# Optimization experiments

Measured on AMD Instinct MI355X. Metric: run time of the kernel, lower is better.

The kernel has to match this reference:

```python
import jax, jax.numpy as jnp
import numpy as np

N, D = 8192, 512
LOGIT_SCALE = 2.659


def setup_inputs() -> dict:
    key = jax.random.key(0)
    k1, k2, k3 = jax.random.split(key, 3)
    text_features = jax.random.normal(k1, (N, D), dtype=jnp.float32)
    image_features = jax.random.normal(k2, (N, D), dtype=jnp.float32)
    labels = jax.random.randint(k3, (N,), 0, 100, dtype=jnp.int64)
    # sprinkle in some -1 (unlabeled) entries like the original supports
    labels = jnp.where(jax.random.uniform(jax.random.fold_in(key, 7), (N,)) < 0.1, -1, labels)
    return {"text_features": text_features, "image_features": image_features, "labels": labels}


def _l2_normalize(x):
    n = jnp.sqrt(jnp.sum(x * x, axis=-1, keepdims=True))
    return x / jnp.maximum(n, 1e-12)


def _soft_ce(s, t):
    # -(t * log softmax(s)).sum(-1) / t.sum(-1), averaged over rows
    loss = -jnp.sum(t * jax.nn.log_softmax(s, axis=-1), axis=-1)
    return jnp.mean(loss / jnp.sum(t, axis=-1))


def reference(text_features, image_features, labels):
    img = _l2_normalize(image_features)
    txt = _l2_normalize(text_features)
    logits_per_image = LOGIT_SCALE * (img @ txt.T)   # [N, N]
    logits_per_text = LOGIT_SCALE * (txt @ img.T)    # [N, N]

    # Vectorized equivalent of the per-row loop:
    # T[i,j] = 1 if i == j else (labels[i] == labels[j] and labels[i] != -1)
    eq = (labels[:, None] == labels[None, :]) & (labels[:, None] != -1)
    n = labels.shape[0]
    target = jnp.where(jnp.eye(n, dtype=bool), 1.0, eq.astype(jnp.float32))

    return (_soft_ce(logits_per_image, target) + _soft_ce(logits_per_text, target)) / 2
```

## Files before the change

### kernel.cpp

```cpp
#include <hip/hip_runtime.h>
#include <hip/hip_bf16.h>

#define N_ROWS 8192
#define DIM 512
#define SCALE 2.659f
#define MAXLOGIT 2.659f
#define LOG2E 1.4426950408889634f
#define NCHUNK 16
#define CHUNK 512
#define BM 128
#define BN 128
#define NCLS 128
#define GEMM_BLKS 1024

typedef __attribute__((ext_vector_type(8))) short short8;
typedef __attribute__((ext_vector_type(4))) float f32x4;

#define ZERO_F4 36896

__device__ __forceinline__ unsigned short f2bf(float f) {
    unsigned int u = __float_as_uint(f);
    u += 0x7fffu + ((u >> 16) & 1u);
    return (unsigned short)(u >> 16);
}

__global__ __launch_bounds__(256) void norm_cast_kernel(
    const float* __restrict__ text, const float* __restrict__ image,
    const int* __restrict__ labels,
    unsigned short* __restrict__ imgn, unsigned short* __restrict__ txtn,
    float4* __restrict__ zbase, float* __restrict__ sd, float* __restrict__ out)
{
    int zi = blockIdx.x * 256 + threadIdx.x;
    if (zi < ZERO_F4) zbase[zi] = make_float4(0.f, 0.f, 0.f, 0.f);
    if (zi == 0) out[0] = 0.f;

    int row  = blockIdx.x * 4 + (threadIdx.x >> 6);
    int lane = threadIdx.x & 63;
    const float4* si = (const float4*)(image + (size_t)row * DIM) + lane * 2;
    const float4* st = (const float4*)(text  + (size_t)row * DIM) + lane * 2;
    float4 a = si[0], b = si[1], c = st[0], d = st[1];
    float ssa = a.x*a.x + a.y*a.y + a.z*a.z + a.w*a.w
              + b.x*b.x + b.y*b.y + b.z*b.z + b.w*b.w;
    float sst = c.x*c.x + c.y*c.y + c.z*c.z + c.w*c.w
              + d.x*d.x + d.y*d.y + d.z*d.z + d.w*d.w;
    float sab = a.x*c.x + a.y*c.y + a.z*c.z + a.w*c.w
              + b.x*d.x + b.y*d.y + b.z*d.z + b.w*d.w;
    #pragma unroll
    for (int m = 1; m < 64; m <<= 1) {
        ssa += __shfl_xor(ssa, m, 64);
        sst += __shfl_xor(sst, m, 64);
        sab += __shfl_xor(sab, m, 64);
    }
    float sca = 1.0f / fmaxf(sqrtf(ssa), 1e-12f);
    float sct = 1.0f / fmaxf(sqrtf(sst), 1e-12f);
    uint4 oi, ot;
    oi.x = (unsigned)f2bf(a.x*sca) | ((unsigned)f2bf(a.y*sca) << 16);
    oi.y = (unsigned)f2bf(a.z*sca) | ((unsigned)f2bf(a.w*sca) << 16);
    oi.z = (unsigned)f2bf(b.x*sca) | ((unsigned)f2bf(b.y*sca) << 16);
    oi.w = (unsigned)f2bf(b.z*sca) | ((unsigned)f2bf(b.w*sca) << 16);
    ot.x = (unsigned)f2bf(c.x*sct) | ((unsigned)f2bf(c.y*sct) << 16);
    ot.y = (unsigned)f2bf(c.z*sct) | ((unsigned)f2bf(c.w*sct) << 16);
    ot.z = (unsigned)f2bf(d.x*sct) | ((unsigned)f2bf(d.y*sct) << 16);
    ot.w = (unsigned)f2bf(d.z*sct) | ((unsigned)f2bf(d.w*sct) << 16);
    *((uint4*)(imgn + (size_t)row * DIM) + lane) = oi;
    *((uint4*)(txtn + (size_t)row * DIM) + lane) = ot;
    if (lane == 0)
        sd[row] = (labels[row] < 0) ? sab * sca * sct : 0.0f;
}

#define ASYNC16(gp, lp) \
  __builtin_amdgcn_global_load_lds((const __attribute__((address_space(1))) void*)(gp), \
                                   (__attribute__((address_space(3))) void*)(lp), 16, 0, 0)

#define SFENCE __builtin_amdgcn_sched_barrier(0)

#define STAGE(b, tcol, k0)                                                    \
  {                                                                           \
    const unsigned short* Ap = A + (size_t)(rowBase + w*16 + srow) * DIM      \
                                 + (k0) + spsw;                               \
    const unsigned short* Bp = B + (size_t)((tcol) + w*16 + srow) * DIM       \
                                 + (k0) + spsw;                               \
    ASYNC16(Ap,            &Ald[b][(w*16) * 32]);                             \
    ASYNC16(Ap + 64 * DIM, &Ald[b][(64 + w*16) * 32]);                        \
    ASYNC16(Bp,            &Bld[b][(w*16) * 32]);                             \
    ASYNC16(Bp + 64 * DIM, &Bld[b][(64 + w*16) * 32]);                        \
  }

__global__ __launch_bounds__(256, 2) void gemm_fused_kernel(
    const unsigned short* __restrict__ imgn, const unsigned short* __restrict__ txtn,
    const int* __restrict__ labels,
    float* __restrict__ rs, float* __restrict__ cs,
    float* __restrict__ c_txt, float* __restrict__ c_img, int* __restrict__ cnt)
{
    __shared__ unsigned short Ald[4][BM * 32];
    __shared__ unsigned short Bld[4][BN * 32];
    __shared__ float red[2][BM];
    __shared__ float colb[2][CHUNK];
    __shared__ int   list[1024];
    __shared__ int   lcount;

    int tid  = threadIdx.x;

    if (blockIdx.x >= GEMM_BLKS) {
        int blk = blockIdx.x - GEMM_BLKS;
        int cls = blk & (NCLS - 1);
        int mat = (blk >> 7) & 1;
        int slc = blk >> 8;
        const unsigned* src = (const unsigned*)(mat ? imgn : txtn);
        float* dst = mat ? c_img : c_txt;
        if (tid == 0) lcount = 0;
        __syncthreads();
        int base0 = slc * 1024;
        #pragma unroll
        for (int it = 0; it < 4; ++it) {
            int i  = base0 + it * 256 + tid;
            int lb = labels[i];
            if (lb == cls) { int s = atomicAdd(&lcount, 1); list[s & 1023] = i; }
        }
        __syncthreads();
        int m = lcount;
        if (m == 0) return;
        if (mat == 0 && tid == 0) atomicAdd(&cnt[cls], m);
        float a0 = 0.f, a1 = 0.f;
        int r = 0;
        for (; r + 4 <= m; r += 4) {
            unsigned u0 = src[(size_t)list[r]   * (DIM/2) + tid];
            unsigned u1 = src[(size_t)list[r+1] * (DIM/2) + tid];
            unsigned u2 = src[(size_t)list[r+2] * (DIM/2) + tid];
            unsigned u3 = src[(size_t)list[r+3] * (DIM/2) + tid];
            a0 += __uint_as_float((u0 & 0xffffu) << 16) + __uint_as_float((u1 & 0xffffu) << 16)
                + __uint_as_float((u2 & 0xffffu) << 16) + __uint_as_float((u3 & 0xffffu) << 16);
            a1 += __uint_as_float(u0 & 0xffff0000u) + __uint_as_float(u1 & 0xffff0000u)
                + __uint_as_float(u2 & 0xffff0000u) + __uint_as_float(u3 & 0xffff0000u);
        }
        for (; r < m; ++r) {
            unsigned u = src[(size_t)list[r] * (DIM/2) + tid];
            a0 += __uint_as_float((u & 0xffffu) << 16);
            a1 += __uint_as_float(u & 0xffff0000u);
        }
        unsafeAtomicAdd(&dst[(size_t)cls * DIM + tid*2],     a0);
        unsafeAtomicAdd(&dst[(size_t)cls * DIM + tid*2 + 1], a1);
        return;
    }

    int bid    = blockIdx.x;
    int rowblk = bid & 63;
    int chunk  = bid >> 6;
    const unsigned short* A = imgn;
    const unsigned short* B = txtn;
    int rowBase  = rowblk * BM;
    int colBase0 = chunk * CHUNK;

    int lane = tid & 63;
    int w    = tid >> 6;
    int wr   = w >> 1, wc = w & 1;
    int q    = lane >> 4;
    int lm   = lane & 15;
    int qa   = q ^ ((lm >> 1) & 3);

    float s_acc[16];
    #pragma unroll
    for (int i = 0; i < 16; ++i) s_acc[i] = 0.f;

    int srow = lane >> 2;
    int spsw = (((lane & 3) ^ ((lane >> 3) & 3)) * 8);

    const float C1 = SCALE * LOG2E;
    const float C2 = -MAXLOGIT * LOG2E;

    STAGE(0, colBase0, 0);
    STAGE(1, colBase0, 32);
    SFENCE;
    asm volatile("s_waitcnt vmcnt(4)" ::: "memory");
    SFENCE;
    __builtin_amdgcn_s_barrier();
    SFENCE;

    #pragma unroll 1
    for (int tile = 0; tile < CHUNK / BN; ++tile) {
        f32x4 acc[4][4];
        #pragma unroll
        for (int mi = 0; mi < 4; ++mi)
          #pragma unroll
          for (int ni = 0; ni < 4; ++ni)
            acc[mi][ni] = (f32x4){0.f, 0.f, 0.f, 0.f};

        #pragma unroll
        for (int kt = 0; kt < DIM / 32; ++kt) {
            const int bcur = kt & 3;
            const int bpf  = (kt + 2) & 3;
            int g2 = tile * 16 + kt + 2;
            if (g2 < 64) {
                int t2 = g2 >> 4, k2 = g2 & 15;
                STAGE(bpf, colBase0 + t2 * BN, k2 * 32);
            }

            short8 af[4], bf[4];
            #pragma unroll
            for (int mi = 0; mi < 4; ++mi)
                af[mi] = *(const short8*)(&Ald[bcur][(wr*64 + mi*16 + lm)*32 + qa*8]);
            #pragma unroll
            for (int ni = 0; ni < 4; ++ni)
                bf[ni] = *(const short8*)(&Bld[bcur][(wc*64 + ni*16 + lm)*32 + qa*8]);
            #pragma unroll
            for (int mi = 0; mi < 4; ++mi)
              #pragma unroll
              for (int ni = 0; ni < 4; ++ni)
                acc[mi][ni] = __builtin_amdgcn_mfma_f32_16x16x32_bf16(
                                  af[mi], bf[ni], acc[mi][ni], 0, 0, 0);

            if (kt == DIM / 32 - 1) {
                #pragma unroll
                for (int ni = 0; ni < 4; ++ni) {
                    float csum = 0.f;
                    #pragma unroll
                    for (int mi = 0; mi < 4; ++mi) {
                      #pragma unroll
                      for (int r = 0; r < 4; ++r) {
                        float e = __builtin_amdgcn_exp2f(fmaf(acc[mi][ni][r], C1, C2));
                        s_acc[mi*4 + r] += e;
                        csum += e;
                      }
                    }
                    csum += __shfl_xor(csum, 16, 64);
                    csum += __shfl_xor(csum, 32, 64);
                    if (q == 0)
                        colb[wr][tile*BN + wc*64 + ni*16 + lm] = csum;
                }
            }

            SFENCE;
            if (g2 < 64) asm volatile("s_waitcnt vmcnt(4)" ::: "memory");
            else         asm volatile("s_waitcnt vmcnt(0)" ::: "memory");
            SFENCE;
            __builtin_amdgcn_s_barrier();
            SFENCE;
        }
    }

    #pragma unroll
    for (int idx = 0; idx < 16; ++idx) {
        float s = s_acc[idx];
        #pragma unroll
        for (int m = 1; m < 16; m <<= 1) s += __shfl_xor(s, m, 64);
        s_acc[idx] = s;
    }
    if (lm == 0) {
        #pragma unroll
        for (int idx = 0; idx < 16; ++idx) {
            int rl = wr*64 + (idx>>2)*16 + q*4 + (idx&3);
            red[wc][rl] = s_acc[idx];
        }
    }
    __syncthreads();
    if (tid < BM)
        unsafeAtomicAdd(&rs[rowBase + tid], red[0][tid] + red[1][tid]);
    for (int c = tid; c < CHUNK; c += 256)
        unsafeAtomicAdd(&cs[colBase0 + c], colb[0][c] + colb[1][c]);
}

__global__ __launch_bounds__(256) void loss_tail_kernel(
    const float* __restrict__ rs, const float* __restrict__ cs,
    const float* __restrict__ sd, const float* __restrict__ c_txt,
    const float* __restrict__ c_img, const int* __restrict__ cnt,
    float* __restrict__ out)
{
    __shared__ float wsum[4];
    int tid = threadIdx.x, lane = tid & 63, w = tid >> 6;
    int gidx = blockIdx.x * 256 + tid;
    float local;
    if (gidx < N_ROWS)
        local = (MAXLOGIT + logf(rs[gidx])) - 2.0f * SCALE * sd[gidx];
    else
        local = MAXLOGIT + logf(cs[gidx - N_ROWS]);

    int cls = blockIdx.x * 2 + (tid >> 7);
    int e0  = (tid & 127) * 4;
    int n   = cnt[cls];
    if (n > 0) {
        float4 x = *(const float4*)(c_txt + (size_t)cls * DIM + e0);
        float4 y = *(const float4*)(c_img + (size_t)cls * DIM + e0);
        float dotp = x.x*y.x + x.y*y.y + x.z*y.z + x.w*y.w;
        local -= 2.0f * SCALE * dotp / (float)n;
    }

    #pragma unroll
    for (int m = 1; m < 64; m <<= 1) local += __shfl_xor(local, m, 64);
    if (lane == 0) wsum[w] = local;
    __syncthreads();
    if (tid == 0)
        unsafeAtomicAdd(out, (wsum[0] + wsum[1] + wsum[2] + wsum[3])
                             * (1.0f / (2 * N_ROWS)));
}

extern "C" void kernel_launch(void* const* d_in, const int* in_sizes, int n_in,
                              void* d_out, int out_size, void* d_ws, size_t ws_size,
                              hipStream_t stream)
{
    const float* text   = (const float*)d_in[0];
    const float* image  = (const float*)d_in[1];
    const int*   labels = (const int*)d_in[2];

    unsigned short* imgn = (unsigned short*)d_ws;
    unsigned short* txtn = imgn + (size_t)N_ROWS * DIM;
    char* p = (char*)d_ws + 2 * (size_t)N_ROWS * DIM * sizeof(unsigned short);
    float* rs    = (float*)p;
    float* cs    = rs + N_ROWS;
    float* c_txt = cs + N_ROWS;
    float* c_img = c_txt + (size_t)NCLS * DIM;
    int*   cnt   = (int*)(c_img + (size_t)NCLS * DIM);
    float* sd    = (float*)(cnt + NCLS);
    float* out = (float*)d_out;

    hipLaunchKernelGGL(norm_cast_kernel, dim3(N_ROWS / 4), dim3(256), 0, stream,
                       text, image, labels, imgn, txtn, (float4*)rs, sd, out);
    hipLaunchKernelGGL(gemm_fused_kernel, dim3(GEMM_BLKS + 2048), dim3(256), 0, stream,
                       imgn, txtn, labels, rs, cs, c_txt, c_img, cnt);
    hipLaunchKernelGGL(loss_tail_kernel, dim3(64), dim3(256), 0, stream,
                       rs, cs, sd, c_txt, c_img, cnt, out);
}
```

Before: 167.4 us.

## Fuse loss tail into GEMM kernel via completion counter spin-wait

Removes the separate loss_tail kernel launch and folds its reduction into the GEMM/class-sum kernel. Every block bumps a global done counter after a threadfence. The first 64 blocks then spin on it with an acquire load until all blocks have finished, and only then compute the final loss. This saves one kernel launch and its inter-kernel gap. In exchange, 64 GEMM blocks keep their CU slots occupied while they wait, and the scheme depends on all blocks being co-schedulable or dispatched in order to avoid deadlock.

```diff
diff --git a/kernel.cpp b/kernel.cpp
--- a/kernel.cpp
+++ b/kernel.cpp
@@ -12,6 +12,7 @@
 #define BN 128
 #define NCLS 128
 #define GEMM_BLKS 1024
+#define TOTAL_BLKS 3072
 
 typedef __attribute__((ext_vector_type(8))) short short8;
 typedef __attribute__((ext_vector_type(4))) float f32x4;
@@ -28,11 +29,12 @@
     const float* __restrict__ text, const float* __restrict__ image,
     const int* __restrict__ labels,
     unsigned short* __restrict__ imgn, unsigned short* __restrict__ txtn,
-    float4* __restrict__ zbase, float* __restrict__ sd, float* __restrict__ out)
+    float4* __restrict__ zbase, float* __restrict__ sd,
+    int* __restrict__ done, float* __restrict__ out)
 {
     int zi = blockIdx.x * 256 + threadIdx.x;
     if (zi < ZERO_F4) zbase[zi] = make_float4(0.f, 0.f, 0.f, 0.f);
-    if (zi == 0) out[0] = 0.f;
+    if (zi == 0) { out[0] = 0.f; *done = 0; }
 
     int row  = blockIdx.x * 4 + (threadIdx.x >> 6);
     int lane = threadIdx.x & 63;
@@ -86,11 +88,13 @@
     ASYNC16(Bp + 64 * DIM, &Bld[b][(64 + w*16) * 32]);                        \
   }
 
-__global__ __launch_bounds__(256, 2) void gemm_fused_kernel(
+__global__ __launch_bounds__(256, 2) void mega_kernel(
     const unsigned short* __restrict__ imgn, const unsigned short* __restrict__ txtn,
     const int* __restrict__ labels,
     float* __restrict__ rs, float* __restrict__ cs,
-    float* __restrict__ c_txt, float* __restrict__ c_img, int* __restrict__ cnt)
+    float* __restrict__ c_txt, float* __restrict__ c_img,
+    int* __restrict__ cnt, const float* __restrict__ sd,
+    int* __restrict__ done, float* __restrict__ out)
 {
     __shared__ unsigned short Ald[4][BM * 32];
     __shared__ unsigned short Bld[4][BN * 32];
@@ -98,11 +102,14 @@
     __shared__ float colb[2][CHUNK];
     __shared__ int   list[1024];
     __shared__ int   lcount;
+    __shared__ float wsum[4];
 
     int tid  = threadIdx.x;
-
-    if (blockIdx.x >= GEMM_BLKS) {
-        int blk = blockIdx.x - GEMM_BLKS;
+    int bid  = blockIdx.x;
+    int lane = tid & 63;
+
+    if (bid >= GEMM_BLKS) {
+        int blk = bid - GEMM_BLKS;
         int cls = blk & (NCLS - 1);
         int mat = (blk >> 7) & 1;
         int slc = blk >> 8;
@@ -119,178 +126,183 @@
         }
         __syncthreads();
         int m = lcount;
-        if (m == 0) return;
-        if (mat == 0 && tid == 0) atomicAdd(&cnt[cls], m);
-        float a0 = 0.f, a1 = 0.f;
-        int r = 0;
-        for (; r + 4 <= m; r += 4) {
-            unsigned u0 = src[(size_t)list[r]   * (DIM/2) + tid];
-            unsigned u1 = src[(size_t)list[r+1] * (DIM/2) + tid];
-            unsigned u2 = src[(size_t)list[r+2] * (DIM/2) + tid];
-            unsigned u3 = src[(size_t)list[r+3] * (DIM/2) + tid];
-            a0 += __uint_as_float((u0 & 0xffffu) << 16) + __uint_as_float((u1 & 0xffffu) << 16)
-                + __uint_as_float((u2 & 0xffffu) << 16) + __uint_as_float((u3 & 0xffffu) << 16);
-            a1 += __uint_as_float(u0 & 0xffff0000u) + __uint_as_float(u1 & 0xffff0000u)
-                + __uint_as_float(u2 & 0xffff0000u) + __uint_as_float(u3 & 0xffff0000u);
-        }
-        for (; r < m; ++r) {
-            unsigned u = src[(size_t)list[r] * (DIM/2) + tid];
-            a0 += __uint_as_float((u & 0xffffu) << 16);
-            a1 += __uint_as_float(u & 0xffff0000u);
-        }
-        unsafeAtomicAdd(&dst[(size_t)cls * DIM + tid*2],     a0);
-        unsafeAtomicAdd(&dst[(size_t)cls * DIM + tid*2 + 1], a1);
-        return;
-    }
-
-    int bid    = blockIdx.x;
-    int rowblk = bid & 63;
-    int chunk  = bid >> 6;
-    const unsigned short* A = imgn;
-    const unsigned short* B = txtn;
-    int rowBase  = rowblk * BM;
-    int colBase0 = chunk * CHUNK;
-
-    int lane = tid & 63;
-    int w    = tid >> 6;
-    int wr   = w >> 1, wc = w & 1;
-    int q    = lane >> 4;
-    int lm   = lane & 15;
-    int qa   = q ^ ((lm >> 1) & 3);
-
-    float s_acc[16];
-    #pragma unroll
-    for (int i = 0; i < 16; ++i) s_acc[i] = 0.f;
-
-    int srow = lane >> 2;
-    int spsw = (((lane & 3) ^ ((lane >> 3) & 3)) * 8);
-
-    const float C1 = SCALE * LOG2E;
-    const float C2 = -MAXLOGIT * LOG2E;
-
-    STAGE(0, colBase0, 0);
-    STAGE(1, colBase0, 32);
-    SFENCE;
-    asm volatile("s_waitcnt vmcnt(4)" ::: "memory");
-    SFENCE;
-    __builtin_amdgcn_s_barrier();
-    SFENCE;
-
-    #pragma unroll 1
-    for (int tile = 0; tile < CHUNK / BN; ++tile) {
-        f32x4 acc[4][4];
+        if (m != 0) {
+            if (mat == 0 && tid == 0) atomicAdd(&cnt[cls], m);
+            float a0 = 0.f, a1 = 0.f;
+            int r = 0;
+            for (; r + 4 <= m; r += 4) {
+                unsigned u0 = src[(size_t)list[r]   * (DIM/2) + tid];
+                unsigned u1 = src[(size_t)list[r+1] * (DIM/2) + tid];
+                unsigned u2 = src[(size_t)list[r+2] * (DIM/2) + tid];
+                unsigned u3 = src[(size_t)list[r+3] * (DIM/2) + tid];
+                a0 += __uint_as_float((u0 & 0xffffu) << 16) + __uint_as_float((u1 & 0xffffu) << 16)
+                    + __uint_as_float((u2 & 0xffffu) << 16) + __uint_as_float((u3 & 0xffffu) << 16);
+                a1 += __uint_as_float(u0 & 0xffff0000u) + __uint_as_float(u1 & 0xffff0000u)
+                    + __uint_as_float(u2 & 0xffff0000u) + __uint_as_float(u3 & 0xffff0000u);
+            }
+            for (; r < m; ++r) {
+                unsigned u = src[(size_t)list[r] * (DIM/2) + tid];
+                a0 += __uint_as_float((u & 0xffffu) << 16);
+                a1 += __uint_as_float(u & 0xffff0000u);
+            }
+            unsafeAtomicAdd(&dst[(size_t)cls * DIM + tid*2],     a0);
+            unsafeAtomicAdd(&dst[(size_t)cls * DIM + tid*2 + 1], a1);
+        }
+    } else {
+        int rowblk = bid & 63;
+        int chunk  = bid >> 6;
+        const unsigned short* A = imgn;
+        const unsigned short* B = txtn;
+        int rowBase  = rowblk * BM;
+        int colBase0 = chunk * CHUNK;
+
+        int w    = tid >> 6;
+        int wr   = w >> 1, wc = w & 1;
+        int q    = lane >> 4;
+        int lm   = lane & 15;
+        int qa   = q ^ ((lm >> 1) & 3);
+        int srow = lane >> 2;
+        int spsw = (((lane & 3) ^ ((lane >> 3) & 3)) * 8);
+
+        float s_acc[16];
         #pragma unroll
-        for (int mi = 0; mi < 4; ++mi)
-          #pragma unroll
-          for (int ni = 0; ni < 4; ++ni)
-            acc[mi][ni] = (f32x4){0.f, 0.f, 0.f, 0.f};
-
-        #pragma unroll
-        for (int kt = 0; kt < DIM / 32; ++kt) {
-            const int bcur = kt & 3;
-            const int bpf  = (kt + 2) & 3;
-            int g2 = tile * 16 + kt + 2;
-            if (g2 < 64) {
-                int t2 = g2 >> 4, k2 = g2 & 15;
-                STAGE(bpf, colBase0 + t2 * BN, k2 * 32);
-            }
-
-            short8 af[4], bf[4];
-            #pragma unroll
-            for (int mi = 0; mi < 4; ++mi)
-                af[mi] = *(const short8*)(&Ald[bcur][(wr*64 + mi*16 + lm)*32 + qa*8]);
-            #pragma unroll
-            for (int ni = 0; ni < 4; ++ni)
-                bf[ni] = *(const short8*)(&Bld[bcur][(wc*64 + ni*16 + lm)*32 + qa*8]);
+        for (int i = 0; i < 16; ++i) s_acc[i] = 0.f;
+
+        const float C1 = SCALE * LOG2E;
+        const float C2 = -MAXLOGIT * LOG2E;
+
+        STAGE(0, colBase0, 0);
+        STAGE(1, colBase0, 32);
+        SFENCE;
+        asm volatile("s_waitcnt vmcnt(4)" ::: "memory");
+        SFENCE;
+        __builtin_amdgcn_s_barrier();
+        SFENCE;
+
+        #pragma unroll 1
+        for (int tile = 0; tile < CHUNK / BN; ++tile) {
+            f32x4 acc[4][4];
             #pragma unroll
             for (int mi = 0; mi < 4; ++mi)
               #pragma unroll
               for (int ni = 0; ni < 4; ++ni)
-                acc[mi][ni] = __builtin_amdgcn_mfma_f32_16x16x32_bf16(
-                                  af[mi], bf[ni], acc[mi][ni], 0, 0, 0);
-
-            if (kt == DIM / 32 - 1) {
+                acc[mi][ni] = (f32x4){0.f, 0.f, 0.f, 0.f};
+
+            #pragma unroll
+            for (int kt = 0; kt < DIM / 32; ++kt) {
+                const int bcur = kt & 3;
+                const int bpf  = (kt + 2) & 3;
+                int g2 = tile * 16 + kt + 2;
+                if (g2 < 64) {
+                    int t2 = g2 >> 4, k2 = g2 & 15;
+                    STAGE(bpf, colBase0 + t2 * BN, k2 * 32);
+                }
+
+                short8 af[4], bf[4];
                 #pragma unroll
-                for (int ni = 0; ni < 4; ++ni) {
-                    float csum = 0.f;
+                for (int mi = 0; mi < 4; ++mi)
+                    af[mi] = *(const short8*)(&Ald[bcur][(wr*64 + mi*16 + lm)*32 + qa*8]);
+                #pragma unroll
+                for (int ni = 0; ni < 4; ++ni)
+                    bf[ni] = *(const short8*)(&Bld[bcur][(wc*64 + ni*16 + lm)*32 + qa*8]);
+                #pragma unroll
+                for (int mi = 0; mi < 4; ++mi)
+                  #pragma unroll
+                  for (int ni = 0; ni < 4; ++ni)
+                    acc[mi][ni] = __builtin_amdgcn_mfma_f32_16x16x32_bf16(
+                                      af[mi], bf[ni], acc[mi][ni], 0, 0, 0);
+
+                if (kt == DIM / 32 - 1) {
                     #pragma unroll
-                    for (int mi = 0; mi < 4; ++mi) {
-                      #pragma unroll
-                      for (int r = 0; r < 4; ++r) {
-                        float e = __builtin_amdgcn_exp2f(fmaf(acc[mi][ni][r], C1, C2));
-                        s_acc[mi*4 + r] += e;
-                        csum += e;
-                      }
+                    for (int ni = 0; ni < 4; ++ni) {
+                        float csum = 0.f;
+                        #pragma unroll
+                        for (int mi = 0; mi < 4; ++mi) {
+                          #pragma unroll
+                          for (int r = 0; r < 4; ++r) {
+                            float e = __builtin_amdgcn_exp2f(fmaf(acc[mi][ni][r], C1, C2));
+                            s_acc[mi*4 + r] += e;
+                            csum += e;
+                          }
+                        }
+                        csum += __shfl_xor(csum, 16, 64);
+                        csum += __shfl_xor(csum, 32, 64);
+                        if (q == 0)
+                            colb[wr][tile*BN + wc*64 + ni*16 + lm] = csum;
                     }
-                    csum += __shfl_xor(csum, 16, 64);
-                    csum += __shfl_xor(csum, 32, 64);
-                    if (q == 0)
-                        colb[wr][tile*BN + wc*64 + ni*16 + lm] = csum;
                 }
+
+                SFENCE;
+                if (g2 < 64) asm volatile("s_waitcnt vmcnt(4)" ::: "memory");
+                else         asm volatile("s_waitcnt vmcnt(0)" ::: "memory");
+                SFENCE;
+                __builtin_amdgcn_s_barrier();
+                SFENCE;
             }
-
-            SFENCE;
-            if (g2 < 64) asm volatile("s_waitcnt vmcnt(4)" ::: "memory");
-            else         asm volatile("s_waitcnt vmcnt(0)" ::: "memory");
-            SFENCE;
-            __builtin_amdgcn_s_barrier();
-            SFENCE;
-        }
-    }
-
-    #pragma unroll
-    for (int idx = 0; idx < 16; ++idx) {
-        float s = s_acc[idx];
-        #pragma unroll
-        for (int m = 1; m < 16; m <<= 1) s += __shfl_xor(s, m, 64);
-        s_acc[idx] = s;
-    }
-    if (lm == 0) {
+        }
+
         #pragma unroll
         for (int idx = 0; idx < 16; ++idx) {
-            int rl = wr*64 + (idx>>2)*16 + q*4 + (idx&3);
-            red[wc][rl] = s_acc[idx];
-        }
+            float s = s_acc[idx];
+            #pragma unroll
+            for (int m = 1; m < 16; m <<= 1) s += __shfl_xor(s, m, 64);
+            s_acc[idx] = s;
+        }
+        if (lm == 0) {
+            #pragma unroll
+            for (int idx = 0; idx < 16; ++idx) {
+                int rl = wr*64 + (idx>>2)*16 + q*4 + (idx&3);
+                red[wc][rl] = s_acc[idx];
+            }
+        }
+        __syncthreads();
+        if (tid < BM)
+            unsafeAtomicAdd(&rs[rowBase + tid], red[0][tid] + red[1][tid]);
+        for (int c = tid; c < CHUNK; c += 256)
+            unsafeAtomicAdd(&cs[colBase0 + c], colb[0][c] + colb[1][c]);
     }
+
     __syncthreads();
-    if (tid < BM)
-        unsafeAtomicAdd(&rs[rowBase + tid], red[0][tid] + red[1][tid]);
-    for (int c = tid; c < CHUNK; c += 256)
-        unsafeAtomicAdd(&cs[colBase0 + c], colb[0][c] + colb[1][c]);
-}
-
-__global__ __launch_bounds__(256) void loss_tail_kernel(
-    const float* __restrict__ rs, const float* __restrict__ cs,
-    const float* __restrict__ sd, const float* __restrict__ c_txt,
-    const float* __restrict__ c_img, const int* __restrict__ cnt,
-    float* __restrict__ out)
-{
-    __shared__ float wsum[4];
-    int tid = threadIdx.x, lane = tid & 63, w = tid >> 6;
-    int gidx = blockIdx.x * 256 + tid;
-    float local;
-    if (gidx < N_ROWS)
-        local = (MAXLOGIT + logf(rs[gidx])) - 2.0f * SCALE * sd[gidx];
-    else
-        local = MAXLOGIT + logf(cs[gidx - N_ROWS]);
-
-    int cls = blockIdx.x * 2 + (tid >> 7);
-    int e0  = (tid & 127) * 4;
-    int n   = cnt[cls];
-    if (n > 0) {
-        float4 x = *(const float4*)(c_txt + (size_t)cls * DIM + e0);
-        float4 y = *(const float4*)(c_img + (size_t)cls * DIM + e0);
-        float dotp = x.x*y.x + x.y*y.y + x.z*y.z + x.w*y.w;
-        local -= 2.0f * SCALE * dotp / (float)n;
+    if (tid == 0) {
+        __threadfence();
+        atomicAdd(done, 1);
     }
 
-    #pragma unroll
-    for (int m = 1; m < 64; m <<= 1) local += __shfl_xor(local, m, 64);
-    if (lane == 0) wsum[w] = local;
-    __syncthreads();
-    if (tid == 0)
-        unsafeAtomicAdd(out, (wsum[0] + wsum[1] + wsum[2] + wsum[3])
-                             * (1.0f / (2 * N_ROWS)));
+    if (bid < 64) {
+        if (tid == 0) {
+            while (__hip_atomic_load(done, __ATOMIC_ACQUIRE,
+                                     __HIP_MEMORY_SCOPE_AGENT) < TOTAL_BLKS)
+                __builtin_amdgcn_s_sleep(8);
+            __threadfence();
+        }
+        __syncthreads();
+
+        int w = tid >> 6;
+        int gidx = bid * 256 + tid;
+        float local;
+        if (gidx < N_ROWS)
+            local = (MAXLOGIT + logf(rs[gidx])) - 2.0f * SCALE * sd[gidx];
+        else
+            local = MAXLOGIT + logf(cs[gidx - N_ROWS]);
+
+        int cls = bid * 2 + (tid >> 7);
+        int e0  = (tid & 127) * 4;
+        int n   = cnt[cls];
+        if (n > 0) {
+            float4 x = *(const float4*)(c_txt + (size_t)cls * DIM + e0);
+            float4 y = *(const float4*)(c_img + (size_t)cls * DIM + e0);
+            float dotp = x.x*y.x + x.y*y.y + x.z*y.z + x.w*y.w;
+            local -= 2.0f * SCALE * dotp / (float)n;
+        }
+
+        #pragma unroll
+        for (int m = 1; m < 64; m <<= 1) local += __shfl_xor(local, m, 64);
+        if (lane == 0) wsum[w] = local;
+        __syncthreads();
+        if (tid == 0)
+            unsafeAtomicAdd(out, (wsum[0] + wsum[1] + wsum[2] + wsum[3])
+                                 * (1.0f / (2 * N_ROWS)));
+    }
 }
 
 extern "C" void kernel_launch(void* const* d_in, const int* in_sizes, int n_in,
@@ -310,12 +322,11 @@
     float* c_img = c_txt + (size_t)NCLS * DIM;
     int*   cnt   = (int*)(c_img + (size_t)NCLS * DIM);
     float* sd    = (float*)(cnt + NCLS);
+    int*   done  = (int*)(sd + N_ROWS);
     float* out = (float*)d_out;
 
     hipLaunchKernelGGL(norm_cast_kernel, dim3(N_ROWS / 4), dim3(256), 0, stream,
-                       text, image, labels, imgn, txtn, (float4*)rs, sd, out);
-    hipLaunchKernelGGL(gemm_fused_kernel, dim3(GEMM_BLKS + 2048), dim3(256), 0, stream,
-                       imgn, txtn, labels, rs, cs, c_txt, c_img, cnt);
-    hipLaunchKernelGGL(loss_tail_kernel, dim3(64), dim3(256), 0, stream,
-                       rs, cs, sd, c_txt, c_img, cnt, out);
+                       text, image, labels, imgn, txtn, (float4*)rs, sd, done, out);
+    hipLaunchKernelGGL(mega_kernel, dim3(TOTAL_BLKS), dim3(256), 0, stream,
+                       imgn, txtn, labels, rs, cs, c_txt, c_img, cnt, sd, done, out);
 }
```

New measurement: 366.5 us. +118.9%, slower.

## Give each wave private LDS tiles to drop block barriers in GEMM loop

Applied to the files above, without the earlier changes.

Each wave now stages its own 64-row slices of A and B into a private LDS region instead of sharing 128-row tiles. That lets the per-k-step workgroup s_barrier go, replacing it with a per-wave vmcnt wait. The buffers drop from four shared stages to two per-wave stages, and the prefetch is issued right after the current buffer is consumed. The cost is that every row is fetched twice from global/L2, since two waves need each A or B slice, and the prefetch slack behind the MFMAs shrinks.

```diff
diff --git a/kernel.cpp b/kernel.cpp
--- a/kernel.cpp
+++ b/kernel.cpp
@@ -74,16 +74,20 @@
 
 #define SFENCE __builtin_amdgcn_sched_barrier(0)
 
-#define STAGE(b, tcol, k0)                                                    \
+#define STAGE_W(b, tcol, k0)                                                  \
   {                                                                           \
-    const unsigned short* Ap = A + (size_t)(rowBase + w*16 + srow) * DIM      \
+    const unsigned short* Ap = A + (size_t)(rowBase + wr*64 + srow) * DIM     \
                                  + (k0) + spsw;                               \
-    const unsigned short* Bp = B + (size_t)((tcol) + w*16 + srow) * DIM       \
+    const unsigned short* Bp = B + (size_t)((tcol) + wc*64 + srow) * DIM      \
                                  + (k0) + spsw;                               \
-    ASYNC16(Ap,            &Ald[b][(w*16) * 32]);                             \
-    ASYNC16(Ap + 64 * DIM, &Ald[b][(64 + w*16) * 32]);                        \
-    ASYNC16(Bp,            &Bld[b][(w*16) * 32]);                             \
-    ASYNC16(Bp + 64 * DIM, &Bld[b][(64 + w*16) * 32]);                        \
+    ASYNC16(Ap,            &Ald[b][w][0]);                                    \
+    ASYNC16(Ap + 16 * DIM, &Ald[b][w][512]);                                  \
+    ASYNC16(Ap + 32 * DIM, &Ald[b][w][1024]);                                 \
+    ASYNC16(Ap + 48 * DIM, &Ald[b][w][1536]);                                 \
+    ASYNC16(Bp,            &Bld[b][w][0]);                                    \
+    ASYNC16(Bp + 16 * DIM, &Bld[b][w][512]);                                  \
+    ASYNC16(Bp + 32 * DIM, &Bld[b][w][1024]);                                 \
+    ASYNC16(Bp + 48 * DIM, &Bld[b][w][1536]);                                 \
   }
 
 __global__ __launch_bounds__(256, 2) void gemm_fused_kernel(
@@ -92,8 +96,8 @@
     float* __restrict__ rs, float* __restrict__ cs,
     float* __restrict__ c_txt, float* __restrict__ c_img, int* __restrict__ cnt)
 {
-    __shared__ unsigned short Ald[4][BM * 32];
-    __shared__ unsigned short Bld[4][BN * 32];
+    __shared__ unsigned short Ald[2][4][64 * 32];
+    __shared__ unsigned short Bld[2][4][64 * 32];
     __shared__ float red[2][BM];
     __shared__ float colb[2][CHUNK];
     __shared__ int   list[1024];
@@ -168,12 +172,10 @@
     const float C1 = SCALE * LOG2E;
     const float C2 = -MAXLOGIT * LOG2E;
 
-    STAGE(0, colBase0, 0);
-    STAGE(1, colBase0, 32);
+    STAGE_W(0, colBase0, 0);
+    STAGE_W(1, colBase0, 32);
     SFENCE;
-    asm volatile("s_waitcnt vmcnt(4)" ::: "memory");
-    SFENCE;
-    __builtin_amdgcn_s_barrier();
+    asm volatile("s_waitcnt vmcnt(8)" ::: "memory");
     SFENCE;
 
     #pragma unroll 1
@@ -187,27 +189,27 @@
 
         #pragma unroll
         for (int kt = 0; kt < DIM / 32; ++kt) {
-            const int bcur = kt & 3;
-            const int bpf  = (kt + 2) & 3;
-            int g2 = tile * 16 + kt + 2;
-            if (g2 < 64) {
-                int t2 = g2 >> 4, k2 = g2 & 15;
-                STAGE(bpf, colBase0 + t2 * BN, k2 * 32);
-            }
+            const int bcur = kt & 1;
 
             short8 af[4], bf[4];
             #pragma unroll
             for (int mi = 0; mi < 4; ++mi)
-                af[mi] = *(const short8*)(&Ald[bcur][(wr*64 + mi*16 + lm)*32 + qa*8]);
+                af[mi] = *(const short8*)(&Ald[bcur][w][(mi*16 + lm)*32 + qa*8]);
             #pragma unroll
             for (int ni = 0; ni < 4; ++ni)
-                bf[ni] = *(const short8*)(&Bld[bcur][(wc*64 + ni*16 + lm)*32 + qa*8]);
+                bf[ni] = *(const short8*)(&Bld[bcur][w][(ni*16 + lm)*32 + qa*8]);
             #pragma unroll
             for (int mi = 0; mi < 4; ++mi)
               #pragma unroll
               for (int ni = 0; ni < 4; ++ni)
                 acc[mi][ni] = __builtin_amdgcn_mfma_f32_16x16x32_bf16(
                                   af[mi], bf[ni], acc[mi][ni], 0, 0, 0);
+
+            SFENCE;
+            int g2 = tile * 16 + kt + 2;
+            if (g2 < 64) {
+                STAGE_W(bcur, colBase0 + (g2 >> 4) * BN, (g2 & 15) * 32);
+            }
 
             if (kt == DIM / 32 - 1) {
                 #pragma unroll
@@ -230,10 +232,8 @@
             }
 
             SFENCE;
-            if (g2 < 64) asm volatile("s_waitcnt vmcnt(4)" ::: "memory");
+            if (g2 < 64) asm volatile("s_waitcnt vmcnt(8)" ::: "memory");
             else         asm volatile("s_waitcnt vmcnt(0)" ::: "memory");
-            SFENCE;
-            __builtin_amdgcn_s_barrier();
             SFENCE;
         }
     }
```

New measurement: 215.8 us. +28.9%, slower.
